# Kernel tuning notes

Measured on AMD Instinct MI355X. Metric: run time of the kernel, lower is better.

The kernel has to match this reference:

```python
import jax, jax.numpy as jnp
import numpy as np

BOX_SIDE = 50.0  # orthorhombic simulation cell side length


def setup_inputs() -> dict:
    key = jax.random.key(0)
    k1, _ = jax.random.split(key)
    N = 8192
    pos = jax.random.uniform(k1, (N, 3), dtype=jnp.float32) * BOX_SIDE  # cartesian positions in box
    box = jnp.ones((3,), dtype=jnp.float32) * BOX_SIDE                   # box lengths (orthorhombic)
    return {"pos": pos, "box": box, "k": 17}


def reference(pos, box, k):
    """Periodic (minimum-image) k-NN graph: returns (edge_index [2, N*k], knn_dist [N, k])."""
    N = pos.shape[0]
    # Accumulate squared wrapped distances one spatial dim at a time to avoid an (N,N,3) intermediate.
    d2 = jnp.zeros((N, N), dtype=pos.dtype)
    for d in range(pos.shape[1]):  # fixed small loop over 3 spatial dims
        diff = pos[:, None, d] - pos[None, :, d]
        diff = diff - box[d] * jnp.round(diff / box[d])  # minimum-image wrap
        d2 = d2 + diff * diff
    # Exclude self-edges.
    d2 = jnp.where(jnp.eye(N, dtype=bool), jnp.inf, d2)
    # k nearest neighbors per node (smallest distance => top_k of negated d2).
    _, idx = jax.lax.top_k(-d2, k)                      # idx: [N, k]
    knn_d2 = jnp.take_along_axis(d2, idx, axis=1)       # [N, k]
    knn_dist = jnp.sqrt(knn_d2)
    src = jnp.repeat(jnp.arange(N), k)
    edge_index = jnp.stack([src, idx.reshape(-1)])      # [2, N*k] (source, neighbor)
    return edge_index, knn_dist
```

## Files before the change

kernel.cpp:

```cpp
#include <hip/hip_runtime.h>
#include <math.h>

#define K 17
#define WAVE 64
#define G 10
#define CELLS (G*G*G)
#define BCAP 16
#define OVCAP 128
#define CAP 128
#define KEY_MAX 0xFFFFFFFFFFFFFFFFULL

__device__ __forceinline__ bool lex_less(float ad, int ai, float bd, int bi) {
    return (ad < bd) || (ad == bd && ai < bi);
}


__global__ __launch_bounds__(256) void prep_bucket(
    const float* __restrict__ pos, const float* __restrict__ box,
    int* __restrict__ cnt, int* __restrict__ ovCnt,
    float4* __restrict__ ov, float4* __restrict__ bucket, int N)
{
    const int t = blockIdx.x * 256 + threadIdx.x;
    if (t >= N) return;
    const float x = pos[3*t+0], y = pos[3*t+1], z = pos[3*t+2];
    const float invx = (float)G / box[0];
    const float invy = (float)G / box[1];
    const float invz = (float)G / box[2];
    const int cx = min((int)(x * invx), G-1);
    const int cy = min((int)(y * invy), G-1);
    const int cz = min((int)(z * invz), G-1);
    const int cell = (cz*G + cy)*G + cx;
    const int slot = atomicAdd(&cnt[cell], 1);
    const float4 v = make_float4(x, y, z, __int_as_float(t));
    if (slot < BCAP) bucket[cell*BCAP + slot] = v;
    else {
        int o = atomicAdd(ovCnt, 1);
        if (o < OVCAP) ov[o] = v;
    }
}


__global__ __launch_bounds__(256, 4) void knn_main(
    const float* __restrict__ pos, const float* __restrict__ box,
    const int* __restrict__ cnt, const int* __restrict__ ovCnt,
    const float4* __restrict__ ov, const float4* __restrict__ bucket,
    float* __restrict__ out, int N)
{
    const int lane = threadIdx.x & 63;
    const int wid  = threadIdx.x >> 6;
    const int i = blockIdx.x * 4 + wid;
    if (i >= N) return;

    __shared__ unsigned long long surv[4][CAP];

    const float bx = box[0], by = box[1], bz = box[2];
    const float hx = 0.5f*bx, hy = 0.5f*by, hz = 0.5f*bz;
    const float invx = (float)G/bx, invy = (float)G/by, invz = (float)G/bz;
    const float cmin = fminf(bx, fminf(by, bz)) / (float)G;

    const float xi = pos[3*i+0], yi = pos[3*i+1], zi = pos[3*i+2];
    const int cx = min((int)(xi*invx), G-1);
    const int cy = min((int)(yi*invy), G-1);
    const int cz = min((int)(zi*invz), G-1);

    const long kN = (long)N * K;
    const int slot = lane & 15;
    const int gq   = lane >> 4;

    int  M = 0;
    bool have = false;

    int  base = 0;
    bool bad  = false;

    auto flush = [&](unsigned long long key, unsigned long long tk) {
        const bool sv = (key <= tk);
        unsigned long long mk = __ballot(sv);
        int pc = __popcll(mk);
        if (base + pc <= CAP) {
            if (sv) {
                int below = __popcll(mk & ((1ULL << lane) - 1ULL));
                surv[wid][base + below] = key;
            }
        } else bad = true;
        base += pc;
    };

    auto round_mi = [&](float4 pnt, bool valid, unsigned long long tk) {
        unsigned long long key = KEY_MAX;
        const int j = __float_as_int(pnt.w);
        if (valid && j != i) {
            float dx = __fsub_rn(xi, pnt.x);
            float dy = __fsub_rn(yi, pnt.y);
            float dz = __fsub_rn(zi, pnt.z);
            dx = dx > hx ? __fsub_rn(dx, bx) : (dx < -hx ? __fadd_rn(dx, bx) : dx);
            dy = dy > hy ? __fsub_rn(dy, by) : (dy < -hy ? __fadd_rn(dy, by) : dy);
            dz = dz > hz ? __fsub_rn(dz, bz) : (dz < -hz ? __fadd_rn(dz, bz) : dz);
            float cd = __fadd_rn(__fadd_rn(__fmul_rn(dx, dx), __fmul_rn(dy, dy)),
                                 __fmul_rn(dz, dz));
            key = ((unsigned long long)__float_as_uint(cd) << 13) | (unsigned)j;
        }
        flush(key, tk);
    };

    {
        const int oc = ovCnt[0];
        float4 pv[7]; int cv[7]; bool gv[7];
        float wox[7], woy[7], woz[7];
#pragma unroll
        for (int p = 0; p < 7; ++p) {
            const int g = 4*p + gq;
            gv[p] = (g < 27);
            int cell = 0; float wx = 0.f, wy = 0.f, wz = 0.f;
            if (gv[p]) {
                int ox = g % 3 - 1, oy = (g/3) % 3 - 1, oz = g/9 - 1;
                int ux = cx + ox;
                if (ux < 0)       { ux += G; wx =  bx; }
                else if (ux >= G) { ux -= G; wx = -bx; }
                int uy = cy + oy;
                if (uy < 0)       { uy += G; wy =  by; }
                else if (uy >= G) { uy -= G; wy = -by; }
                int uz = cz + oz;
                if (uz < 0)       { uz += G; wz =  bz; }
                else if (uz >= G) { uz -= G; wz = -bz; }
                cell = (uz*G + uy)*G + ux;
            }
            cv[p] = cnt[cell];
            pv[p] = bucket[cell*BCAP + slot];
            wox[p] = wx; woy[p] = wy; woz[p] = wz;
        }
        float4 ov0 = ov[lane];
        float4 ov1 = ov[WAVE + lane];

        bool vm[7];
#pragma unroll
        for (int p = 0; p < 7; ++p) vm[p] = gv[p] && (slot < min(cv[p], BCAP));

        const float thr = cmin * cmin * 0.999f;
        const unsigned long long thrKey =
            ((unsigned long long)__float_as_uint(thr) << 13) | 0x1FFFULL;

        base = 0; bad = (oc > OVCAP);
#pragma unroll
        for (int p = 0; p < 7; ++p) {
            unsigned long long key = KEY_MAX;
            const float4 pnt = pv[p];
            const int j = __float_as_int(pnt.w);
            if (vm[p] && j != i) {
                float dx = __fadd_rn(__fsub_rn(xi, pnt.x), wox[p]);
                float dy = __fadd_rn(__fsub_rn(yi, pnt.y), woy[p]);
                float dz = __fadd_rn(__fsub_rn(zi, pnt.z), woz[p]);
                float cd = __fadd_rn(__fadd_rn(__fmul_rn(dx, dx), __fmul_rn(dy, dy)),
                                     __fmul_rn(dz, dz));
                key = ((unsigned long long)__float_as_uint(cd) << 13) | (unsigned)j;
            }
            flush(key, thrKey);
        }
        if (oc > 0) {
            round_mi(ov0, lane < oc, thrKey);
            round_mi(ov1, WAVE + lane < oc, thrKey);
        }
        if (!bad && base >= K) { have = true; M = base; }
    }

    if (!have && ovCnt[0] <= OVCAP) {
        const int oc = ovCnt[0];
        const float thr2 = cmin * cmin * 1.9580f;
        const unsigned long long thrKey2 =
            ((unsigned long long)__float_as_uint(thr2) << 13) | 0x1FFFULL;

        base = 0; bad = false;
#pragma unroll 1
        for (int b = 0; b < 4; ++b) {
            float4 pv2[8]; int cv2[8]; bool gv2[8];
            float wx2[8], wy2[8], wz2[8];
#pragma unroll
            for (int q = 0; q < 8; ++q) {
                const int g = 4*(8*b + q) + gq;
                gv2[q] = (g < 125);
                int cell = 0; float wx = 0.f, wy = 0.f, wz = 0.f;
                if (gv2[q]) {
                    int ox = g % 5 - 2, oy = (g/5) % 5 - 2, oz = g/25 - 2;
                    int ux = cx + ox;
                    if (ux < 0)       { ux += G; wx =  bx; }
                    else if (ux >= G) { ux -= G; wx = -bx; }
                    int uy = cy + oy;
                    if (uy < 0)       { uy += G; wy =  by; }
                    else if (uy >= G) { uy -= G; wy = -by; }
                    int uz = cz + oz;
                    if (uz < 0)       { uz += G; wz =  bz; }
                    else if (uz >= G) { uz -= G; wz = -bz; }
                    cell = (uz*G + uy)*G + ux;
                }
                cv2[q] = cnt[cell];
                pv2[q] = bucket[cell*BCAP + slot];
                wx2[q] = wx; wy2[q] = wy; wz2[q] = wz;
            }
#pragma unroll
            for (int q = 0; q < 8; ++q) {
                unsigned long long key = KEY_MAX;
                const float4 pnt = pv2[q];
                const int j = __float_as_int(pnt.w);
                if (gv2[q] && (slot < min(cv2[q], BCAP)) && j != i) {
                    float dx = __fadd_rn(__fsub_rn(xi, pnt.x), wx2[q]);
                    float dy = __fadd_rn(__fsub_rn(yi, pnt.y), wy2[q]);
                    float dz = __fadd_rn(__fsub_rn(zi, pnt.z), wz2[q]);
                    float cd = __fadd_rn(__fadd_rn(__fmul_rn(dx, dx), __fmul_rn(dy, dy)),
                                         __fmul_rn(dz, dz));
                    key = ((unsigned long long)__float_as_uint(cd) << 13) | (unsigned)j;
                }
                flush(key, thrKey2);
            }
        }
        if (!bad && oc > 0) {
            round_mi(ov[lane],        lane < oc,        thrKey2);
            round_mi(ov[WAVE + lane], WAVE + lane < oc, thrKey2);
        }
        if (!bad && base >= K) { have = true; M = base; }
    }

    if (have) {
        __asm__ __volatile__("s_waitcnt lgkmcnt(0)" ::: "memory");
        unsigned long long k0 = surv[wid][(lane < M) ? lane : 0];
        unsigned long long k1 = (lane + 64 < M) ? surv[wid][lane + 64] : KEY_MAX;
        int r0 = 0, r1 = 0;
#pragma unroll 2
        for (int m = 0; m < M; ++m) {
            unsigned long long s = surv[wid][m];
            r0 += (s < k0) ? 1 : 0;
            r1 += (s < k1) ? 1 : 0;
        }
        if (lane < K) out[(long)i*K + lane] = (float)i;
        if (lane < M && r0 < K) {
            out[kN + (long)i*K + r0]   = (float)(int)(k0 & 0x1FFFULL);
            out[2*kN + (long)i*K + r0] = __fsqrt_rn(__uint_as_float((unsigned)(k0 >> 13)));
        }
        if (lane + 64 < M && r1 < K) {
            out[kN + (long)i*K + r1]   = (float)(int)(k1 & 0x1FFFULL);
            out[2*kN + (long)i*K + r1] = __fsqrt_rn(__uint_as_float((unsigned)(k1 >> 13)));
        }
        return;
    }

    {
        float d[K]; int id[K];
#pragma unroll
        for (int m = 0; m < K; ++m) { d[m] = INFINITY; id[m] = 0x7fffffff; }

#pragma unroll 1
        for (int j0 = 0; j0 < N; j0 += WAVE) {
            const int j = j0 + lane;
            float cd = INFINITY; int ci = 0x7fffffff;
            if (j < N && j != i) {
                float dx = __fsub_rn(xi, pos[3*j+0]);
                float dy = __fsub_rn(yi, pos[3*j+1]);
                float dz = __fsub_rn(zi, pos[3*j+2]);
                dx = dx > hx ? __fsub_rn(dx, bx) : (dx < -hx ? __fadd_rn(dx, bx) : dx);
                dy = dy > hy ? __fsub_rn(dy, by) : (dy < -hy ? __fadd_rn(dy, by) : dy);
                dz = dz > hz ? __fsub_rn(dz, bz) : (dz < -hz ? __fadd_rn(dz, bz) : dz);
                cd = __fadd_rn(__fadd_rn(__fmul_rn(dx, dx), __fmul_rn(dy, dy)),
                               __fmul_rn(dz, dz));
                ci = j;
            }
            if (lex_less(cd, ci, d[K-1], id[K-1])) {
                bool lt[K];
#pragma unroll
                for (int m = 0; m < K; ++m) lt[m] = lex_less(cd, ci, d[m], id[m]);
#pragma unroll
                for (int m = K-1; m >= 1; --m) {
                    d[m]  = lt[m-1] ? d[m-1]  : (lt[m] ? cd : d[m]);
                    id[m] = lt[m-1] ? id[m-1] : (lt[m] ? ci : id[m]);
                }
                d[0]  = lt[0] ? cd : d[0];
                id[0] = lt[0] ? ci : id[0];
            }
        }

#pragma unroll 1
        for (int e = 0; e < K; ++e) {
            float bv = d[0]; int bi = id[0];
#pragma unroll
            for (int off = 32; off >= 1; off >>= 1) {
                float ov2 = __shfl_xor(bv, off, WAVE);
                int   oi = __shfl_xor(bi, off, WAVE);
                if (lex_less(ov2, oi, bv, bi)) { bv = ov2; bi = oi; }
            }
            if (d[0] == bv && id[0] == bi) {
#pragma unroll
                for (int m = 0; m < K-1; ++m) { d[m] = d[m+1]; id[m] = id[m+1]; }
                d[K-1] = INFINITY; id[K-1] = 0x7fffffff;
            }
            if (lane == e) {
                out[kN + (long)i*K + e]   = (float)bi;
                out[2*kN + (long)i*K + e] = __fsqrt_rn(bv);
            }
        }
        if (lane < K) out[(long)i*K + lane] = (float)i;
    }
}

extern "C" void kernel_launch(void* const* d_in, const int* in_sizes, int n_in,
                              void* d_out, int out_size, void* d_ws, size_t ws_size,
                              hipStream_t stream) {
    const float* pos = (const float*)d_in[0];
    const float* box = (const float*)d_in[1];
    const int N = in_sizes[0] / 3;

    unsigned char* ws = (unsigned char*)d_ws;
    int*    cnt    = (int*)ws;
    int*    ovCnt  = (int*)(ws + 4000);
    float4* ov     = (float4*)(ws + 4096);
    float4* bucket = (float4*)(ws + 8192);

    hipMemsetAsync(cnt, 0, 4004, stream);
    prep_bucket<<<dim3((N + 255) / 256), dim3(256), 0, stream>>>(
        pos, box, cnt, ovCnt, ov, bucket, N);
    knn_main<<<dim3((N + 3) / 4), dim3(256), 0, stream>>>(
        pos, box, cnt, ovCnt, ov, bucket, (float*)d_out, N);
}
```

Before: 85.56 us.

## Move brute-force fallback to separate kernel and fold overflow into cell slots

The exact brute-force k-NN fallback is moved out of the main kernel into a separate knn_exact kernel that processes a compacted list of failed points, recorded with an atomic counter. The aim is to cut register pressure and code size in the main kernel. The first cell-search round now uses its unused 28th slot to load the first 16 overflow entries and skips the remaining overflow loads when counts are small. The rank-counting loop now reads survivor keys in pairs. In exchange it adds a third kernel launch and more workspace, and the fallback runs on only 64 blocks.

```diff
diff --git a/kernel.cpp b/kernel.cpp
--- a/kernel.cpp
+++ b/kernel.cpp
@@ -44,6 +44,7 @@
     const float* __restrict__ pos, const float* __restrict__ box,
     const int* __restrict__ cnt, const int* __restrict__ ovCnt,
     const float4* __restrict__ ov, const float4* __restrict__ bucket,
+    int* __restrict__ failCnt, int* __restrict__ failList,
     float* __restrict__ out, int N)
 {
     const int lane = threadIdx.x & 63;
@@ -103,16 +104,17 @@
         flush(key, tk);
     };
 
+    const int oc = ovCnt[0];
+
     {
-        const int oc = ovCnt[0];
-        float4 pv[7]; int cv[7]; bool gv[7];
-        float wox[7], woy[7], woz[7];
+        float4 pv[7]; int cv[7];
+        float wox[6], woy[6], woz[6];
 #pragma unroll
         for (int p = 0; p < 7; ++p) {
             const int g = 4*p + gq;
-            gv[p] = (g < 27);
+            const bool isOv = (p == 6) && (gq == 3);
             int cell = 0; float wx = 0.f, wy = 0.f, wz = 0.f;
-            if (gv[p]) {
+            if (!isOv) {
                 int ox = g % 3 - 1, oy = (g/3) % 3 - 1, oz = g/9 - 1;
                 int ux = cx + ox;
                 if (ux < 0)       { ux += G; wx =  bx; }
@@ -125,16 +127,10 @@
                 else if (uz >= G) { uz -= G; wz = -bz; }
                 cell = (uz*G + uy)*G + ux;
             }
-            cv[p] = cnt[cell];
-            pv[p] = bucket[cell*BCAP + slot];
-            wox[p] = wx; woy[p] = wy; woz[p] = wz;
-        }
-        float4 ov0 = ov[lane];
-        float4 ov1 = ov[WAVE + lane];
-
-        bool vm[7];
-#pragma unroll
-        for (int p = 0; p < 7; ++p) vm[p] = gv[p] && (slot < min(cv[p], BCAP));
+            if (isOv) { cv[p] = oc; pv[p] = ov[slot]; }
+            else      { cv[p] = cnt[cell]; pv[p] = bucket[cell*BCAP + slot]; }
+            if (p < 6) { wox[p] = wx; woy[p] = wy; woz[p] = wz; }
+        }
 
         const float thr = cmin * cmin * 0.999f;
         const unsigned long long thrKey =
@@ -142,11 +138,11 @@
 
         base = 0; bad = (oc > OVCAP);
 #pragma unroll
-        for (int p = 0; p < 7; ++p) {
+        for (int p = 0; p < 6; ++p) {
             unsigned long long key = KEY_MAX;
             const float4 pnt = pv[p];
             const int j = __float_as_int(pnt.w);
-            if (vm[p] && j != i) {
+            if ((slot < min(cv[p], BCAP)) && j != i) {
                 float dx = __fadd_rn(__fsub_rn(xi, pnt.x), wox[p]);
                 float dy = __fadd_rn(__fsub_rn(yi, pnt.y), woy[p]);
                 float dz = __fadd_rn(__fsub_rn(zi, pnt.z), woz[p]);
@@ -156,15 +152,16 @@
             }
             flush(key, thrKey);
         }
-        if (oc > 0) {
-            round_mi(ov0, lane < oc, thrKey);
-            round_mi(ov1, WAVE + lane < oc, thrKey);
+        round_mi(pv[6], slot < min(cv[6], BCAP), thrKey);
+        if (oc > 16) {
+            round_mi(ov[min(16 + lane, OVCAP-1)], 16 + lane < oc, thrKey);
+            if (oc > 80)
+                round_mi(ov[min(80 + lane, OVCAP-1)], 80 + lane < oc, thrKey);
         }
         if (!bad && base >= K) { have = true; M = base; }
     }
 
-    if (!have && ovCnt[0] <= OVCAP) {
-        const int oc = ovCnt[0];
+    if (!have && oc <= OVCAP) {
         const float thr2 = cmin * cmin * 1.9580f;
         const unsigned long long thrKey2 =
             ((unsigned long long)__float_as_uint(thr2) << 13) | 0x1FFFULL;
@@ -213,22 +210,28 @@
             }
         }
         if (!bad && oc > 0) {
-            round_mi(ov[lane],        lane < oc,        thrKey2);
-            round_mi(ov[WAVE + lane], WAVE + lane < oc, thrKey2);
+            round_mi(ov[lane], lane < oc, thrKey2);
+            if (oc > WAVE)
+                round_mi(ov[WAVE + lane], WAVE + lane < oc, thrKey2);
         }
         if (!bad && base >= K) { have = true; M = base; }
     }
 
     if (have) {
+        if (lane == 0 && (M & 1)) surv[wid][M] = KEY_MAX;
         __asm__ __volatile__("s_waitcnt lgkmcnt(0)" ::: "memory");
         unsigned long long k0 = surv[wid][(lane < M) ? lane : 0];
         unsigned long long k1 = (lane + 64 < M) ? surv[wid][lane + 64] : KEY_MAX;
         int r0 = 0, r1 = 0;
+        const int Me = (M + 1) & ~1;
 #pragma unroll 2
-        for (int m = 0; m < M; ++m) {
-            unsigned long long s = surv[wid][m];
-            r0 += (s < k0) ? 1 : 0;
-            r1 += (s < k1) ? 1 : 0;
+        for (int m = 0; m < Me; m += 2) {
+            const ulonglong2 s2 =
+                *reinterpret_cast<const ulonglong2*>(&surv[wid][m]);
+            r0 += (s2.x < k0) ? 1 : 0;
+            r1 += (s2.x < k1) ? 1 : 0;
+            r0 += (s2.y < k0) ? 1 : 0;
+            r1 += (s2.y < k1) ? 1 : 0;
         }
         if (lane < K) out[(long)i*K + lane] = (float)i;
         if (lane < M && r0 < K) {
@@ -242,7 +245,32 @@
         return;
     }
 
-    {
+    if (lane == 0) {
+        int f = atomicAdd(failCnt, 1);
+        if (f < N) failList[f] = i;
+    }
+}
+
+
+__global__ __launch_bounds__(256) void knn_exact(
+    const float* __restrict__ pos, const float* __restrict__ box,
+    const int* __restrict__ failCnt, const int* __restrict__ failList,
+    float* __restrict__ out, int N)
+{
+    const int lane = threadIdx.x & 63;
+    const int gw = (blockIdx.x * 256 + threadIdx.x) >> 6;
+    const int nw = (gridDim.x * 256) >> 6;
+    const int fc = min(failCnt[0], N);
+    if (fc == 0) return;
+
+    const float bx = box[0], by = box[1], bz = box[2];
+    const float hx = 0.5f*bx, hy = 0.5f*by, hz = 0.5f*bz;
+    const long kN = (long)N * K;
+
+    for (int f = gw; f < fc; f += nw) {
+        const int i = failList[f];
+        const float xi = pos[3*i+0], yi = pos[3*i+1], zi = pos[3*i+2];
+
         float d[K]; int id[K];
 #pragma unroll
         for (int m = 0; m < K; ++m) { d[m] = INFINITY; id[m] = 0x7fffffff; }
@@ -307,14 +335,18 @@
     const int N = in_sizes[0] / 3;
 
     unsigned char* ws = (unsigned char*)d_ws;
-    int*    cnt    = (int*)ws;
-    int*    ovCnt  = (int*)(ws + 4000);
-    float4* ov     = (float4*)(ws + 4096);
-    float4* bucket = (float4*)(ws + 8192);
-
-    hipMemsetAsync(cnt, 0, 4004, stream);
+    int*    cnt      = (int*)ws;
+    int*    ovCnt    = (int*)(ws + 4000);
+    int*    failCnt  = (int*)(ws + 4004);
+    float4* ov       = (float4*)(ws + 4096);
+    float4* bucket   = (float4*)(ws + 8192);
+    int*    failList = (int*)(ws + 270336);
+
+    hipMemsetAsync(cnt, 0, 4008, stream);
     prep_bucket<<<dim3((N + 255) / 256), dim3(256), 0, stream>>>(
         pos, box, cnt, ovCnt, ov, bucket, N);
     knn_main<<<dim3((N + 3) / 4), dim3(256), 0, stream>>>(
-        pos, box, cnt, ovCnt, ov, bucket, (float*)d_out, N);
-}
+        pos, box, cnt, ovCnt, ov, bucket, failCnt, failList, (float*)d_out, N);
+    knn_exact<<<dim3(64), dim3(256), 0, stream>>>(
+        pos, box, failCnt, failList, (float*)d_out, N);
+}
```

Result: no change. 85.76 us (+0.2%).
